# Kernel tuning notes

Measured on AMD Instinct MI355X. Metric: run time of the kernel, lower is better.

Reference implementation:

```python
import jax, jax.numpy as jnp
import numpy as np

jax.config.update("jax_enable_x64", True)

NNZ = 8_388_608        # number of sparse (feature_id, value) pairs
N_FEATURES = 8_192     # number of calibrated feature ids
N_BIN = 63             # bin boundaries per feature -> 64 bins
OUT_BITS = 22          # output id space = 1 << 22
GOLDEN32 = np.uint32(0x9E3779B9)  # Knuth multiplicative-hashing constant


def setup_inputs() -> dict:
    key = jax.random.key(0)
    k1, k2, k3 = jax.random.split(key, 3)
    input_keys = jax.random.randint(k1, (NNZ,), 0, 2 * N_FEATURES, dtype=jnp.int64)
    input_vals = jax.random.normal(k2, (NNZ,), dtype=jnp.float32)
    # Calibrated feature ids (sorted) and per-feature sorted bin boundaries.
    feature_ids = jnp.arange(N_FEATURES, dtype=jnp.int64)
    bin_vals = jnp.sort(
        jax.random.normal(k3, (N_FEATURES, N_BIN), dtype=jnp.float32), axis=1
    ).reshape(-1)
    return {
        "input_keys": input_keys,
        "input_vals": input_vals,
        "feature_ids": feature_ids,
        "bin_vals": bin_vals,
    }


def _lower_bound_bins(bin_vals_flat, feat_idx, vals, n_bin):
    """Per-value branchless binary search: bin = sum(bin_row < val).

    bin_vals_flat: [F * n_bin] row-sorted boundaries, feat_idx: [nnz] int,
    vals: [nnz] float. Returns [nnz] int32 bin index in [0, n_bin].
    """
    steps = int(np.ceil(np.log2(n_bin + 1)))  # 6 for n_bin=63
    base = feat_idx.astype(jnp.int64) * n_bin
    lo = jnp.zeros(vals.shape, dtype=jnp.int32)
    hi = jnp.full(vals.shape, n_bin, dtype=jnp.int32)
    for _ in range(steps):
        mid = (lo + hi) >> 1                       # in [0, n_bin]
        mid_safe = jnp.minimum(mid, n_bin - 1)     # gather-safe
        bv = bin_vals_flat[base + mid_safe]
        valid = lo < hi
        go_right = valid & (bv < vals)             # strict '<' => lower bound
        lo = jnp.where(go_right, mid + 1, lo)
        hi = jnp.where(valid & ~go_right, mid, hi)
    return lo


def reference(input_keys, input_vals, feature_ids, bin_vals):
    F = feature_ids.shape[0]
    n_bin = bin_vals.shape[0] // F
    mask = jnp.int64((1 << OUT_BITS) - 1)

    # --- find each key in the (sorted) calibrated feature-id table ---
    idx = jnp.searchsorted(feature_ids, input_keys)          # [nnz]
    idx_safe = jnp.minimum(idx, F - 1)
    calibrated = feature_ids[idx_safe] == input_keys          # [nnz] bool

    # --- bin assignment: bin = sum(bin_vals_row < val) ---
    bins = _lower_bound_bins(bin_vals, idx_safe, input_vals, n_bin)

    # --- 32-bit integer multiplicative hash of (feature_id, bin) ---
    h = (input_keys.astype(jnp.uint32) * GOLDEN32 + bins.astype(jnp.uint32)) * GOLDEN32
    hashed_key = h.astype(jnp.int64) & mask

    out_keys = jnp.where(calibrated, hashed_key, input_keys & mask)
    out_vals = jnp.where(calibrated, jnp.ones_like(input_vals), input_vals)
    # dense_shape of the resulting SparseTensor is [batch, 1 << OUT_BITS]
    return out_keys, out_vals
```

## Files before the change

### kernel.cpp

```cpp
#include <hip/hip_runtime.h>
#include <stdint.h>
#include <math.h>


#define GOLDEN   0x9E3779B9u
#define OUT_MASK ((1u << 22) - 1u)
#define NBIN  63
#define QROW  64
#define NKEY  16384
#define NPIV  8192
#define MASKW (NKEY / 32)

typedef float fx4 __attribute__((ext_vector_type(4)));
typedef int   ix4 __attribute__((ext_vector_type(4)));

__global__ __launch_bounds__(512) void clear_mask_kernel(unsigned* __restrict__ gmask) {
    const int t = threadIdx.x;
    if (t < MASKW) gmask[t] = 0u;
}

__global__ __launch_bounds__(256) void build_tables_kernel(
    const int* __restrict__ fids, const float* __restrict__ bins,
    float* __restrict__ qtab, uint4* __restrict__ gpiv,
    unsigned* __restrict__ gmask, int F)
{
    const int t = blockIdx.x * blockDim.x + threadIdx.x;
    if (t >= F * QROW) return;
    const int r = t >> 6;
    const int j = t & 63;
    const float* src = bins + (size_t)r * NBIN;
    qtab[t] = (j < NBIN) ? src[j] : INFINITY;
    if (j == 0) {
        const int k = fids[r];
        if ((unsigned)k < (unsigned)NKEY) {
            atomicOr(&gmask[k >> 5], 1u << (k & 31));
            if ((unsigned)k < (unsigned)NPIV) {
                uint4 p;
                p.x = __float_as_uint(src[15]);
                p.y = __float_as_uint(src[31]);
                p.z = __float_as_uint(src[47]);
                p.w = (unsigned)r;
                gpiv[k] = p;
            }
        }
    }
}

__device__ __forceinline__ void hd_fallback(
    int k, float v, const int* __restrict__ fids, const float* __restrict__ bins,
    int F, int fsteps, float& okey, float& oval)
{
    int lo = 0, hi = F;
    for (int s = 0; s < fsteps; ++s) {
        int  mid  = (lo + hi) >> 1;
        int  mids = min(mid, F - 1);
        int  fv   = fids[mids];
        bool valid = lo < hi;
        bool right = valid && (fv < k);
        lo = right ? mid + 1 : lo;
        hi = (valid && !right) ? mid : hi;
    }
    const int  idx_safe   = min(lo, F - 1);
    const bool calibrated = (fids[idx_safe] == k);
    const float* brow = bins + (size_t)idx_safe * NBIN;
    int blo = 0, bhi = NBIN;
    #pragma unroll
    for (int s = 0; s < 6; ++s) {
        int   mid  = (blo + bhi) >> 1;
        int   mids = min(mid, NBIN - 1);
        float bv   = brow[mids];
        bool  valid = blo < bhi;
        bool  right = valid && (bv < v);
        blo = right ? mid + 1 : blo;
        bhi = (valid && !right) ? mid : bhi;
    }
    const uint32_t h = ((uint32_t)k * GOLDEN + (uint32_t)blo) * GOLDEN;
    okey = calibrated ? (float)(h & OUT_MASK) : (float)((uint32_t)k & OUT_MASK);
    oval = calibrated ? 1.0f : v;
}

__global__ __launch_bounds__(1024) void hd_main_kernel(
    const int* __restrict__ keys, const float* __restrict__ vals,
    const int* __restrict__ fids, const float* __restrict__ bins,
    const float* __restrict__ qtab, const uint4* __restrict__ gpiv,
    const unsigned* __restrict__ gmask,
    float* __restrict__ out_keys, float* __restrict__ out_vals,
    int n, int F, int fsteps)
{
    extern __shared__ char smem[];
    uint4*    spiv  = reinterpret_cast<uint4*>(smem);
    unsigned* smask = reinterpret_cast<unsigned*>(smem + (size_t)NPIV * sizeof(uint4));

    const int tid = threadIdx.x;
    for (int i = tid; i < NPIV; i += (int)blockDim.x) spiv[i] = gpiv[i];
    if (tid < MASKW) smask[tid] = gmask[tid];
    __syncthreads();

    const int gid = blockIdx.x * blockDim.x + tid;
    const int i0 = gid * 8;
    if (i0 >= n) return;

    int   ks[8];
    float vs[8];
    const bool full = (i0 + 7 < n);
    if (full) {
        const ix4 ka = __builtin_nontemporal_load(reinterpret_cast<const ix4*>(keys + i0));
        const ix4 kb = __builtin_nontemporal_load(reinterpret_cast<const ix4*>(keys + i0 + 4));
        const fx4 va = __builtin_nontemporal_load(reinterpret_cast<const fx4*>(vals + i0));
        const fx4 vb = __builtin_nontemporal_load(reinterpret_cast<const fx4*>(vals + i0 + 4));
        ks[0]=ka.x; ks[1]=ka.y; ks[2]=ka.z; ks[3]=ka.w;
        ks[4]=kb.x; ks[5]=kb.y; ks[6]=kb.z; ks[7]=kb.w;
        vs[0]=va.x; vs[1]=va.y; vs[2]=va.z; vs[3]=va.w;
        vs[4]=vb.x; vs[5]=vb.y; vs[6]=vb.z; vs[7]=vb.w;
    } else {
        #pragma unroll
        for (int j = 0; j < 8; ++j) {
            int idx = min(i0 + j, n - 1);
            ks[j] = keys[idx];
            vs[j] = vals[idx];
        }
    }

    float ok[8], ov[8];
    #pragma unroll
    for (int j = 0; j < 8; ++j) {
        const int   k = ks[j];
        const float v = vs[j];
        if ((unsigned)k < (unsigned)NKEY) {
            const bool calib = (smask[(unsigned)k >> 5] >> (k & 31)) & 1u;
            if (calib) {
                if ((unsigned)k < (unsigned)NPIV) {
                    const uint4 p = spiv[k];
                    const float p0 = __uint_as_float(p.x);
                    const float p1 = __uint_as_float(p.y);
                    const float p2 = __uint_as_float(p.z);
                    const int q = (p0 < v) + (p1 < v) + (p2 < v);
                    const fx4* blk = reinterpret_cast<const fx4*>(
                        qtab + ((size_t)p.w << 6) + (q << 4));
                    const fx4 b0 = blk[0], b1 = blk[1], b2 = blk[2], b3 = blk[3];
                    const int cnt = 16 * q
                        + (b0.x < v) + (b0.y < v) + (b0.z < v) + (b0.w < v)
                        + (b1.x < v) + (b1.y < v) + (b1.z < v) + (b1.w < v)
                        + (b2.x < v) + (b2.y < v) + (b2.z < v) + (b2.w < v)
                        + (b3.x < v) + (b3.y < v) + (b3.z < v) + (b3.w < v);
                    const uint32_t h = ((uint32_t)k * GOLDEN + (uint32_t)cnt) * GOLDEN;
                    ok[j] = (float)(h & OUT_MASK);
                    ov[j] = 1.0f;
                } else {
                    hd_fallback(k, v, fids, bins, F, fsteps, ok[j], ov[j]);
                }
            } else {
                ok[j] = (float)((uint32_t)k & OUT_MASK);
                ov[j] = v;
            }
        } else {
            hd_fallback(k, v, fids, bins, F, fsteps, ok[j], ov[j]);
        }
    }

    if (full) {
        fx4 a, b;
        a.x=ok[0]; a.y=ok[1]; a.z=ok[2]; a.w=ok[3];
        b.x=ok[4]; b.y=ok[5]; b.z=ok[6]; b.w=ok[7];
        __builtin_nontemporal_store(a, reinterpret_cast<fx4*>(out_keys + i0));
        __builtin_nontemporal_store(b, reinterpret_cast<fx4*>(out_keys + i0 + 4));
        a.x=ov[0]; a.y=ov[1]; a.z=ov[2]; a.w=ov[3];
        b.x=ov[4]; b.y=ov[5]; b.z=ov[6]; b.w=ov[7];
        __builtin_nontemporal_store(a, reinterpret_cast<fx4*>(out_vals + i0));
        __builtin_nontemporal_store(b, reinterpret_cast<fx4*>(out_vals + i0 + 4));
    } else {
        for (int j = 0; j < 8 && i0 + j < n; ++j) {
            out_keys[i0 + j] = ok[j];
            out_vals[i0 + j] = ov[j];
        }
    }
}

__global__ __launch_bounds__(256) void hd_simple_kernel(
    const int* __restrict__ keys, const float* __restrict__ vals,
    const int* __restrict__ fids, const float* __restrict__ bins,
    float* __restrict__ out_keys, float* __restrict__ out_vals,
    int n, int F, int fsteps)
{
    const int gid = blockIdx.x * blockDim.x + threadIdx.x;
    const int i0 = gid * 4;
    if (i0 >= n) return;
    #pragma unroll
    for (int j = 0; j < 4; ++j) {
        int idx = min(i0 + j, n - 1);
        float okey, oval;
        hd_fallback(keys[idx], vals[idx], fids, bins, F, fsteps, okey, oval);
        if (i0 + j < n) { out_keys[i0 + j] = okey; out_vals[i0 + j] = oval; }
    }
}

extern "C" void kernel_launch(void* const* d_in, const int* in_sizes, int n_in,
                              void* d_out, int out_size, void* d_ws, size_t ws_size,
                              hipStream_t stream) {
    const int*   keys = (const int*)d_in[0];
    const float* vals = (const float*)d_in[1];
    const int*   fids = (const int*)d_in[2];
    const float* bins = (const float*)d_in[3];

    const int n = in_sizes[0];
    const int F = in_sizes[2];

    int fsteps = 0;
    while ((1 << fsteps) < F + 1) ++fsteps;

    float* out_keys = (float*)d_out;
    float* out_vals = (float*)d_out + n;

    const size_t qtab_bytes = (size_t)F * QROW * sizeof(float);
    const size_t ws_need    = qtab_bytes + (size_t)NPIV * 16 + (size_t)MASKW * 4;
    const size_t lds_bytes  = (size_t)NPIV * 16 + (size_t)MASKW * 4;

    int max_lds = 0;
    hipDeviceGetAttribute(&max_lds, hipDeviceAttributeMaxSharedMemoryPerBlock, 0);

    const bool fast = (ws_size >= ws_need) && ((size_t)max_lds >= lds_bytes) &&
                      (in_sizes[3] == F * NBIN);

    if (fast) {
        float*    qtab  = (float*)d_ws;
        uint4*    gpiv  = (uint4*)((char*)d_ws + qtab_bytes);
        unsigned* gmask = (unsigned*)((char*)gpiv + (size_t)NPIV * 16);

        clear_mask_kernel<<<1, 512, 0, stream>>>(gmask);
        build_tables_kernel<<<(F * QROW + 255) / 256, 256, 0, stream>>>(
            fids, bins, qtab, gpiv, gmask, F);

        (void)hipFuncSetAttribute(
            reinterpret_cast<const void*>(hd_main_kernel),
            hipFuncAttributeMaxDynamicSharedMemorySize, (int)lds_bytes);

        const int threads = 1024;
        const int grid = (n + threads * 8 - 1) / (threads * 8);
        hd_main_kernel<<<grid, threads, lds_bytes, stream>>>(
            keys, vals, fids, bins, qtab, gpiv, gmask,
            out_keys, out_vals, n, F, fsteps);
    } else {
        const int threads = 256;
        const int grid = (n + threads * 4 - 1) / (threads * 4);
        hd_simple_kernel<<<grid, threads, 0, stream>>>(
            keys, vals, fids, bins, out_keys, out_vals, n, F, fsteps);
    }
}
```

Baseline: 164.7 us.

## Restructure bin table into two-level quad tree to cut per-value loads

The per-feature bin table is rebuilt as 80-float rows. Each 16-bin quarter now holds a 4-float header of sub-pivots followed by four 4-float leaves. The main kernel reads the header, picks one leaf and compares against 4 values, instead of loading and comparing all 16 boundaries. This cuts global memory traffic per lookup from 64 bytes to 32 bytes, at the cost of a second dependent load and a larger table. The mask-clearing kernel is also replaced with hipMemsetAsync.

```diff
diff --git a/kernel.cpp b/kernel.cpp
--- a/kernel.cpp
+++ b/kernel.cpp
@@ -6,18 +6,13 @@
 #define GOLDEN   0x9E3779B9u
 #define OUT_MASK ((1u << 22) - 1u)
 #define NBIN  63
-#define QROW  64
+#define QROWF 80
 #define NKEY  16384
 #define NPIV  8192
 #define MASKW (NKEY / 32)
 
 typedef float fx4 __attribute__((ext_vector_type(4)));
 typedef int   ix4 __attribute__((ext_vector_type(4)));
-
-__global__ __launch_bounds__(512) void clear_mask_kernel(unsigned* __restrict__ gmask) {
-    const int t = threadIdx.x;
-    if (t < MASKW) gmask[t] = 0u;
-}
 
 __global__ __launch_bounds__(256) void build_tables_kernel(
     const int* __restrict__ fids, const float* __restrict__ bins,
@@ -25,11 +20,21 @@
     unsigned* __restrict__ gmask, int F)
 {
     const int t = blockIdx.x * blockDim.x + threadIdx.x;
-    if (t >= F * QROW) return;
-    const int r = t >> 6;
-    const int j = t & 63;
+    if (t >= F * QROWF) return;
+    const int r = t / QROWF;
+    const int j = t - r * QROWF;
+    const int q = j / 20;
+    const int u = j - q * 20;
     const float* src = bins + (size_t)r * NBIN;
-    qtab[t] = (j < NBIN) ? src[j] : INFINITY;
+
+    int bi;
+    if (u < 3)       bi = 16 * q + 4 * u + 3;
+    else if (u == 3) bi = -1;
+    else             bi = 16 * q + (u - 4);
+    float val = (bi >= 0 && bi < NBIN) ? src[bi] : INFINITY;
+    if (u == 3) val = 0.0f;
+    qtab[t] = val;
+
     if (j == 0) {
         const int k = fids[r];
         if ((unsigned)k < (unsigned)NKEY) {
@@ -135,14 +140,12 @@
                     const float p1 = __uint_as_float(p.y);
                     const float p2 = __uint_as_float(p.z);
                     const int q = (p0 < v) + (p1 < v) + (p2 < v);
-                    const fx4* blk = reinterpret_cast<const fx4*>(
-                        qtab + ((size_t)p.w << 6) + (q << 4));
-                    const fx4 b0 = blk[0], b1 = blk[1], b2 = blk[2], b3 = blk[3];
-                    const int cnt = 16 * q
-                        + (b0.x < v) + (b0.y < v) + (b0.z < v) + (b0.w < v)
-                        + (b1.x < v) + (b1.y < v) + (b1.z < v) + (b1.w < v)
-                        + (b2.x < v) + (b2.y < v) + (b2.z < v) + (b2.w < v)
-                        + (b3.x < v) + (b3.y < v) + (b3.z < v) + (b3.w < v);
+                    const float* qbase = qtab + (size_t)p.w * QROWF + q * 20;
+                    const fx4 qh = *reinterpret_cast<const fx4*>(qbase);
+                    const int s = (qh.x < v) + (qh.y < v) + (qh.z < v);
+                    const fx4 leaf = *reinterpret_cast<const fx4*>(qbase + 4 + 4 * s);
+                    const int cnt = 16 * q + 4 * s
+                        + (leaf.x < v) + (leaf.y < v) + (leaf.z < v) + (leaf.w < v);
                     const uint32_t h = ((uint32_t)k * GOLDEN + (uint32_t)cnt) * GOLDEN;
                     ok[j] = (float)(h & OUT_MASK);
                     ov[j] = 1.0f;
@@ -211,7 +214,7 @@
     float* out_keys = (float*)d_out;
     float* out_vals = (float*)d_out + n;
 
-    const size_t qtab_bytes = (size_t)F * QROW * sizeof(float);
+    const size_t qtab_bytes = (size_t)F * QROWF * sizeof(float);
     const size_t ws_need    = qtab_bytes + (size_t)NPIV * 16 + (size_t)MASKW * 4;
     const size_t lds_bytes  = (size_t)NPIV * 16 + (size_t)MASKW * 4;
 
@@ -226,8 +229,8 @@
         uint4*    gpiv  = (uint4*)((char*)d_ws + qtab_bytes);
         unsigned* gmask = (unsigned*)((char*)gpiv + (size_t)NPIV * 16);
 
-        clear_mask_kernel<<<1, 512, 0, stream>>>(gmask);
-        build_tables_kernel<<<(F * QROW + 255) / 256, 256, 0, stream>>>(
+        hipMemsetAsync(gmask, 0, (size_t)MASKW * 4, stream);
+        build_tables_kernel<<<(F * QROWF + 255) / 256, 256, 0, stream>>>(
             fids, bins, qtab, gpiv, gmask, F);
 
         (void)hipFuncSetAttribute(
```

Result: slower. 177.8 us (+7.9%).

## Replace pivot-plus-scan binning with linear-interpolation bucket lookup table

Applied to the files above, without the earlier changes.

The build step now makes, for each feature, a 256-entry byte table indexed by a linear quantisation of the value between the first and last boundary. Each byte encodes either the exact bin, a short 4-wide window to scan, or a flag for a full binary search. The main kernel keeps only a packed 4-byte parameter per feature in LDS instead of 16-byte pivots, and usually resolves the bin with one byte gather plus at most one float4 load. This cuts LDS footprint and global reads per element. In exchange it adds a larger build kernel, dependent gathers, more divergence for hard buckets, and relies on reduced-precision packed parameters being used identically in build and lookup.

```diff
diff --git a/kernel.cpp b/kernel.cpp
--- a/kernel.cpp
+++ b/kernel.cpp
@@ -6,7 +6,6 @@
 #define GOLDEN   0x9E3779B9u
 #define OUT_MASK ((1u << 22) - 1u)
 #define NBIN  63
-#define QROW  64
 #define NKEY  16384
 #define NPIV  8192
 #define MASKW (NKEY / 32)
@@ -14,35 +13,77 @@
 typedef float fx4 __attribute__((ext_vector_type(4)));
 typedef int   ix4 __attribute__((ext_vector_type(4)));
 
-__global__ __launch_bounds__(512) void clear_mask_kernel(unsigned* __restrict__ gmask) {
-    const int t = threadIdx.x;
-    if (t < MASKW) gmask[t] = 0u;
+__device__ __forceinline__ int qidx(float v, float lo, float inv) {
+    float h = floorf((v - lo) * inv);
+    h = fminf(fmaxf(h, -1.0f), 254.0f);
+    return (int)h + 1;
 }
 
 __global__ __launch_bounds__(256) void build_tables_kernel(
     const int* __restrict__ fids, const float* __restrict__ bins,
-    float* __restrict__ qtab, uint4* __restrict__ gpiv,
-    unsigned* __restrict__ gmask, int F)
-{
-    const int t = blockIdx.x * blockDim.x + threadIdx.x;
-    if (t >= F * QROW) return;
-    const int r = t >> 6;
-    const int j = t & 63;
-    const float* src = bins + (size_t)r * NBIN;
-    qtab[t] = (j < NBIN) ? src[j] : INFINITY;
-    if (j == 0) {
-        const int k = fids[r];
-        if ((unsigned)k < (unsigned)NKEY) {
+    float* __restrict__ qtab, unsigned char* __restrict__ stab,
+    unsigned* __restrict__ gparam, unsigned* __restrict__ gmask, int F)
+{
+    __shared__ float    sb[64];
+    __shared__ int      sidx[64];
+    __shared__ unsigned sparam;
+
+    const int r = blockIdx.x;
+    const int tid = threadIdx.x;
+    const int k = fids[r];
+    const bool vk = (unsigned)k < (unsigned)NPIV;
+
+    if (tid < 64)
+        sb[tid] = (tid < NBIN) ? bins[(size_t)r * NBIN + tid] : INFINITY;
+    __syncthreads();
+
+    if (tid == 0) {
+        if ((unsigned)k < (unsigned)NKEY)
             atomicOr(&gmask[k >> 5], 1u << (k & 31));
-            if ((unsigned)k < (unsigned)NPIV) {
-                uint4 p;
-                p.x = __float_as_uint(src[15]);
-                p.y = __float_as_uint(src[31]);
-                p.z = __float_as_uint(src[47]);
-                p.w = (unsigned)r;
-                gpiv[k] = p;
-            }
-        }
+        const float b0 = sb[0], b62 = sb[NBIN - 1];
+        const float invf = 254.0f / (b62 - b0);
+        const unsigned p = (__float_as_uint(b0) & 0xFFFF0000u) |
+                           (__float_as_uint(invf) >> 16);
+        sparam = p;
+        if (vk) gparam[k] = p;
+    }
+    __syncthreads();
+
+    const float lo  = __uint_as_float(sparam & 0xFFFF0000u);
+    const float inv = __uint_as_float(sparam << 16);
+
+    if (tid < 64) {
+        sidx[tid] = (tid < NBIN) ? qidx(sb[tid], lo, inv) : 1000;
+        if (vk) qtab[((size_t)k << 6) + tid] = sb[tid];
+    }
+    __syncthreads();
+
+    if (vk) {
+        const int B = tid;
+        int c_lo = 0, c_hi = NBIN, e_lo = 0, e_hi = NBIN;
+        #pragma unroll
+        for (int it = 0; it < 6; ++it) {
+            {
+                int mid = (c_lo + c_hi) >> 1;
+                bool valid = c_lo < c_hi;
+                bool go = valid && (sidx[mid] < B);
+                c_lo = go ? mid + 1 : c_lo;
+                c_hi = (valid && !go) ? mid : c_hi;
+            }
+            {
+                int mid = (e_lo + e_hi) >> 1;
+                bool valid = e_lo < e_hi;
+                bool go = valid && (sidx[mid] < B + 1);
+                e_lo = go ? mid + 1 : e_lo;
+                e_hi = (valid && !go) ? mid : e_hi;
+            }
+        }
+        const int c = c_lo, m = e_lo - c_lo;
+        unsigned char byte;
+        if (m == 0)      byte = (unsigned char)c;
+        else if (m <= 4) byte = (unsigned char)(0x40 | c);
+        else             byte = 0xC0;
+        stab[((size_t)k << 8) + B] = byte;
     }
 }
 
@@ -79,20 +120,37 @@
     oval = calibrated ? 1.0f : v;
 }
 
-__global__ __launch_bounds__(1024) void hd_main_kernel(
+__device__ __forceinline__ int hd_hard(const float* __restrict__ qtab,
+                                       unsigned uk, float v)
+{
+    const float* row = qtab + ((size_t)uk << 6);
+    int blo = 0, bhi = NBIN;
+    #pragma unroll
+    for (int s = 0; s < 6; ++s) {
+        int   mid  = (blo + bhi) >> 1;
+        float bv   = row[min(mid, NBIN - 1)];
+        bool  valid = blo < bhi;
+        bool  right = valid && (bv < v);
+        blo = right ? mid + 1 : blo;
+        bhi = (valid && !right) ? mid : bhi;
+    }
+    return blo;
+}
+
+__global__ __launch_bounds__(1024, 8) void hd_main_kernel(
     const int* __restrict__ keys, const float* __restrict__ vals,
     const int* __restrict__ fids, const float* __restrict__ bins,
-    const float* __restrict__ qtab, const uint4* __restrict__ gpiv,
-    const unsigned* __restrict__ gmask,
+    const float* __restrict__ qtab, const unsigned char* __restrict__ stab,
+    const unsigned* __restrict__ gparam, const unsigned* __restrict__ gmask,
     float* __restrict__ out_keys, float* __restrict__ out_vals,
     int n, int F, int fsteps)
 {
     extern __shared__ char smem[];
-    uint4*    spiv  = reinterpret_cast<uint4*>(smem);
-    unsigned* smask = reinterpret_cast<unsigned*>(smem + (size_t)NPIV * sizeof(uint4));
+    unsigned* sparam = reinterpret_cast<unsigned*>(smem);
+    unsigned* smask  = reinterpret_cast<unsigned*>(smem + (size_t)NPIV * 4);
 
     const int tid = threadIdx.x;
-    for (int i = tid; i < NPIV; i += (int)blockDim.x) spiv[i] = gpiv[i];
+    for (int i = tid; i < NPIV; i += (int)blockDim.x) sparam[i] = gparam[i];
     if (tid < MASKW) smask[tid] = gmask[tid];
     __syncthreads();
 
@@ -122,39 +180,66 @@
     }
 
     float ok[8], ov[8];
+
     #pragma unroll
-    for (int j = 0; j < 8; ++j) {
-        const int   k = ks[j];
-        const float v = vs[j];
-        if ((unsigned)k < (unsigned)NKEY) {
-            const bool calib = (smask[(unsigned)k >> 5] >> (k & 31)) & 1u;
-            if (calib) {
-                if ((unsigned)k < (unsigned)NPIV) {
-                    const uint4 p = spiv[k];
-                    const float p0 = __uint_as_float(p.x);
-                    const float p1 = __uint_as_float(p.y);
-                    const float p2 = __uint_as_float(p.z);
-                    const int q = (p0 < v) + (p1 < v) + (p2 < v);
-                    const fx4* blk = reinterpret_cast<const fx4*>(
-                        qtab + ((size_t)p.w << 6) + (q << 4));
-                    const fx4 b0 = blk[0], b1 = blk[1], b2 = blk[2], b3 = blk[3];
-                    const int cnt = 16 * q
-                        + (b0.x < v) + (b0.y < v) + (b0.z < v) + (b0.w < v)
-                        + (b1.x < v) + (b1.y < v) + (b1.z < v) + (b1.w < v)
-                        + (b2.x < v) + (b2.y < v) + (b2.z < v) + (b2.w < v)
-                        + (b3.x < v) + (b3.y < v) + (b3.z < v) + (b3.w < v);
-                    const uint32_t h = ((uint32_t)k * GOLDEN + (uint32_t)cnt) * GOLDEN;
-                    ok[j] = (float)(h & OUT_MASK);
-                    ov[j] = 1.0f;
-                } else {
-                    hd_fallback(k, v, fids, bins, F, fsteps, ok[j], ov[j]);
-                }
-            } else {
-                ok[j] = (float)((uint32_t)k & OUT_MASK);
-                ov[j] = v;
-            }
-        } else {
-            hd_fallback(k, v, fids, bins, F, fsteps, ok[j], ov[j]);
+    for (int g = 0; g < 2; ++g) {
+        bool fast[4], fb[4];
+        unsigned uks[4];
+        unsigned char tb[4];
+
+        #pragma unroll
+        for (int j = 0; j < 4; ++j) {
+            const int e = g * 4 + j;
+            const unsigned uk = (unsigned)ks[e];
+            uks[j] = uk;
+            const bool in16  = uk < (unsigned)NKEY;
+            const bool calib = in16 && ((smask[(uk >> 5) & (MASKW - 1)] >> (uk & 31)) & 1u);
+            fast[j] = calib && (uk < (unsigned)NPIV);
+            fb[j]   = (!in16) || (calib && !(uk < (unsigned)NPIV));
+        }
+        unsigned boff[4];
+        #pragma unroll
+        for (int j = 0; j < 4; ++j) {
+            const int e = g * 4 + j;
+            const unsigned uk = fast[j] ? uks[j] : 0u;
+            const unsigned pw = sparam[uk];
+            const float lo  = __uint_as_float(pw & 0xFFFF0000u);
+            const float inv = __uint_as_float(pw << 16);
+            const int idx = qidx(vs[e], lo, inv);
+            boff[j] = (uk << 8) + (unsigned)idx;
+        }
+        #pragma unroll
+        for (int j = 0; j < 4; ++j) tb[j] = stab[boff[j]];
+
+        #pragma unroll
+        for (int j = 0; j < 4; ++j) {
+            const int e = g * 4 + j;
+            const unsigned uk = uks[j];
+            const float v = vs[e];
+            const int code = tb[j] >> 6;
+            const int c    = tb[j] & 63;
+
+            int bin = c;
+            if (fast[j] && code == 1) {
+                const int ws = min(c, 60);
+                const fx4 w = *reinterpret_cast<const fx4*>(
+                    qtab + ((size_t)uk << 6) + ws);
+                bin = ws + (w.x < v) + (w.y < v) + (w.z < v) + (w.w < v);
+            }
+            if (fast[j] && code >= 2) {
+                bin = hd_hard(qtab, uk, v);
+            }
+
+            const uint32_t h = ((uint32_t)uk * GOLDEN + (uint32_t)bin) * GOLDEN;
+            const float fkey = (float)(h & OUT_MASK);
+            const float pkey = (float)(uk & OUT_MASK);
+
+            ok[e] = fast[j] ? fkey : pkey;
+            ov[e] = fast[j] ? 1.0f : v;
+
+            if (fb[j]) {
+                hd_fallback(ks[e], v, fids, bins, F, fsteps, ok[e], ov[e]);
+            }
         }
     }
 
@@ -211,24 +296,27 @@
     float* out_keys = (float*)d_out;
     float* out_vals = (float*)d_out + n;
 
-    const size_t qtab_bytes = (size_t)F * QROW * sizeof(float);
-    const size_t ws_need    = qtab_bytes + (size_t)NPIV * 16 + (size_t)MASKW * 4;
-    const size_t lds_bytes  = (size_t)NPIV * 16 + (size_t)MASKW * 4;
+    const size_t qtab_bytes = (size_t)NPIV * 64 * sizeof(float);
+    const size_t stab_bytes = (size_t)NPIV * 256;
+    const size_t gpar_bytes = (size_t)NPIV * 4;
+    const size_t ws_need    = qtab_bytes + stab_bytes + gpar_bytes + MASKW * 4;
+    const size_t lds_bytes  = (size_t)NPIV * 4 + MASKW * 4;
 
     int max_lds = 0;
     hipDeviceGetAttribute(&max_lds, hipDeviceAttributeMaxSharedMemoryPerBlock, 0);
 
     const bool fast = (ws_size >= ws_need) && ((size_t)max_lds >= lds_bytes) &&
-                      (in_sizes[3] == F * NBIN);
+                      (in_sizes[3] == F * NBIN) && (F <= 65536);
 
     if (fast) {
-        float*    qtab  = (float*)d_ws;
-        uint4*    gpiv  = (uint4*)((char*)d_ws + qtab_bytes);
-        unsigned* gmask = (unsigned*)((char*)gpiv + (size_t)NPIV * 16);
-
-        clear_mask_kernel<<<1, 512, 0, stream>>>(gmask);
-        build_tables_kernel<<<(F * QROW + 255) / 256, 256, 0, stream>>>(
-            fids, bins, qtab, gpiv, gmask, F);
+        float*         qtab   = (float*)d_ws;
+        unsigned char* stab   = (unsigned char*)d_ws + qtab_bytes;
+        unsigned*      gparam = (unsigned*)((char*)d_ws + qtab_bytes + stab_bytes);
+        unsigned*      gmask  = gparam + NPIV;
+
+        hipMemsetAsync(gmask, 0, MASKW * 4, stream);
+        build_tables_kernel<<<F, 256, 0, stream>>>(
+            fids, bins, qtab, stab, gparam, gmask, F);
 
         (void)hipFuncSetAttribute(
             reinterpret_cast<const void*>(hd_main_kernel),
@@ -237,7 +325,7 @@
         const int threads = 1024;
         const int grid = (n + threads * 8 - 1) / (threads * 8);
         hd_main_kernel<<<grid, threads, lds_bytes, stream>>>(
-            keys, vals, fids, bins, qtab, gpiv, gmask,
+            keys, vals, fids, bins, qtab, stab, gparam, gmask,
             out_keys, out_vals, n, F, fsteps);
     } else {
         const int threads = 256;
```

Result: slower. 178.7 us (+8.5%).
